# Kernel tuning notes

Hardware: AMD Instinct MI355X
Metric: run time of the kernel (lower is better)

## Reference

```python
import jax, jax.numpy as jnp
import numpy as np

LAYERS = [3, 1024, 512, 256, 128, 1]
WIDTHS = [3, 1024, 1024, 1024, 1024, 1]  # width per BsPINN: 2^(i-1)*Layers[i]
N = 131072


def _mask(num_blocks, bs1, bs2):
    # block-diagonal mask of ones, built statically (constant under jit)
    return jnp.asarray(np.kron(np.eye(num_blocks, dtype=np.float32),
                               np.ones((bs1, bs2), dtype=np.float32)))


def _xavier(key, shape, fan_in, fan_out):
    lim = np.sqrt(6.0 / (fan_in + fan_out)).astype(np.float32)
    return jax.random.uniform(key, shape, jnp.float32, -lim, lim)


def setup_inputs() -> dict:
    key = jax.random.key(0)
    ks = jax.random.split(key, 6)
    inp = {
        "X": jax.random.uniform(ks[0], (N, 3), dtype=jnp.float32),
        "lb_X": jnp.zeros((3,), jnp.float32),
        "ub_X": jnp.ones((3,), jnp.float32),
    }
    for i in range(5):
        # xavier scale per sub-block Layers[i] x Layers[i+1], as in the torch init
        inp[f"W{i}"] = _xavier(ks[i + 1], (WIDTHS[i], WIDTHS[i + 1]),
                               LAYERS[i], LAYERS[i + 1])
        inp[f"b{i}"] = jnp.zeros((1, WIDTHS[i + 1]), jnp.float32)
    return inp


def reference(X, lb_X, ub_X, W0, b0, W1, b1, W2, b2, W3, b3, W4, b4):
    # masks for hidden layers l=2,3: 2 blocks of 512x512, 4 blocks of 256x256
    m2 = _mask(2, LAYERS[2], 2 * LAYERS[3])   # [1024,1024]
    m3 = _mask(4, LAYERS[3], 2 * LAYERS[4])   # [1024,1024]
    h = 2.0 * (X - lb_X) / (ub_X - lb_X) - 1.0  # [N,3]
    h = jnp.sin(h @ W0 + b0)            # [N,1024] dense
    h = jnp.sin(h @ W1 + b1)            # [N,1024] dense
    h = jnp.sin(h @ (W2 * m2) + b2)     # [N,1024] block-diag (2 blocks)
    h = jnp.sin(h @ (W3 * m3) + b3)     # [N,1024] block-diag (4 blocks)
    return h @ W4 + b4                  # [N,1]
```

## Files before the change

kernel.cpp:

```cpp
#include <hip/hip_runtime.h>

typedef _Float16 f16x8 __attribute__((ext_vector_type(8)));
typedef _Float16 f16x4 __attribute__((ext_vector_type(4)));
typedef __fp16  fp16x2 __attribute__((ext_vector_type(2)));
typedef float f32x4 __attribute__((ext_vector_type(4)));
typedef unsigned int u32;

#define ROWS 64
#define THREADS 1024

__global__ __launch_bounds__(512) void pack_weights(
    const float* __restrict__ W1, const float* __restrict__ W2,
    const float* __restrict__ W3, _Float16* __restrict__ WF1,
    _Float16* __restrict__ WF2, _Float16* __restrict__ WF3) {
  int t = blockIdx.x * 512 + threadIdx.x;
  const float* src; _Float16* dst; int idx, ct, kt, lane, kbase;
  if (t < 131072) {
    idx = t; src = W1; dst = WF1;
    ct = idx >> 11; kt = (idx >> 6) & 31; lane = idx & 63; kbase = 0;
  } else if (t < 196608) {
    idx = t - 131072; src = W2; dst = WF2;
    ct = idx >> 10; kt = (idx >> 6) & 15; lane = idx & 63;
    kbase = (ct >= 32) ? 512 : 0;
  } else {
    idx = t - 196608; src = W3; dst = WF3;
    ct = idx >> 9; kt = (idx >> 6) & 7; lane = idx & 63;
    kbase = (ct >> 4) << 8;
  }
  int c  = ct * 16 + (lane & 15);
  int k0 = kbase + kt * 32 + ((lane >> 4) << 3);
  f16x8 v;
#pragma unroll
  for (int j = 0; j < 8; ++j) v[j] = (_Float16)src[(size_t)(k0 + j) * 1024 + c];
  *reinterpret_cast<f16x8*>(dst + (size_t)idx * 8) = v;
}

template <int KT>
__device__ __forceinline__ void layer_mfma(char* hb, const _Float16* __restrict__ WF,
                                           const float* __restrict__ bias,
                                           int wid, int lane, int kbase) {
  f32x4 acc[4][4];
#pragma unroll
  for (int cf = 0; cf < 4; ++cf)
#pragma unroll
    for (int rf = 0; rf < 4; ++rf) acc[cf][rf] = f32x4{0.f, 0.f, 0.f, 0.f};

  const f16x8* wf = reinterpret_cast<const f16x8*>(WF) +
                    (u32)(wid * 4 * KT * 64 + lane);
  const int arow = lane & 15;
  const int koff = (lane >> 4) << 3;
  const u32 abase = (u32)(arow * 2048);
  const u32 axor  = (u32)((arow & 7) << 4);

#pragma unroll 1
  for (int kt = 0; kt < KT; ++kt) {
    f16x8 w[4];
#pragma unroll
    for (int cf = 0; cf < 4; ++cf)
      w[cf] = wf[(u32)(cf * KT) * 64u + (u32)kt * 64u];
    u32 kb = (u32)((kbase + kt * 32 + koff) * 2);
    f16x8 h[4];
#pragma unroll
    for (int rf = 0; rf < 4; ++rf) {
      u32 addr = ((u32)(rf * 32768) + abase + kb) ^ axor;
      h[rf] = *reinterpret_cast<const f16x8*>(hb + addr);
    }
    __builtin_amdgcn_s_setprio(1);
#pragma unroll
    for (int cf = 0; cf < 4; ++cf)
#pragma unroll
      for (int rf = 0; rf < 4; ++rf)
        acc[cf][rf] = __builtin_amdgcn_mfma_f32_16x16x32_f16(w[cf], h[rf],
                                                             acc[cf][rf], 0, 0, 0);
    __builtin_amdgcn_s_setprio(0);
  }

  __syncthreads();
  const int csub = (lane >> 4) << 2;
  const int rr   = lane & 15;
#pragma unroll
  for (int cf = 0; cf < 4; ++cf) {
    int c0 = wid * 64 + cf * 16 + csub;
    f32x4 bb = *reinterpret_cast<const f32x4*>(bias + c0);
#pragma unroll
    for (int rf = 0; rf < 4; ++rf) {
      int r = rf * 16 + rr;
      float s0 = __sinf(acc[cf][rf][0] + bb[0]);
      float s1 = __sinf(acc[cf][rf][1] + bb[1]);
      float s2 = __sinf(acc[cf][rf][2] + bb[2]);
      float s3 = __sinf(acc[cf][rf][3] + bb[3]);
      union { fp16x2 h2[2]; f16x4 v; } pk;
      pk.h2[0] = __builtin_amdgcn_cvt_pkrtz(s0, s1);
      pk.h2[1] = __builtin_amdgcn_cvt_pkrtz(s2, s3);
      u32 addr = ((u32)(r * 2048 + c0 * 2)) ^ ((u32)((r & 7) << 4));
      *reinterpret_cast<f16x4*>(hb + addr) = pk.v;
    }
  }
  __syncthreads();
}

__global__
__attribute__((amdgpu_flat_work_group_size(1024, 1024), amdgpu_waves_per_eu(4, 4)))
void bspinn_fused(
    const float* __restrict__ X, const float* __restrict__ lb,
    const float* __restrict__ ub,
    const float* __restrict__ W0, const float* __restrict__ b0,
    const _Float16* __restrict__ WF1, const float* __restrict__ b1,
    const _Float16* __restrict__ WF2, const float* __restrict__ b2,
    const _Float16* __restrict__ WF3, const float* __restrict__ b3,
    const float* __restrict__ W4, const float* __restrict__ b4,
    float* __restrict__ out) {
  __shared__ alignas(16) char hb[ROWS * 2048];
  __shared__ float xs[ROWS * 4];
  __shared__ float partials[16 * ROWS];

  const int tid  = threadIdx.x;
  const int lane = tid & 63;
  const int wid  = tid >> 6;
  const int r0   = blockIdx.x * ROWS;

  if (tid < ROWS * 3) {
    int r = tid / 3, j = tid - r * 3;
    float x = X[(size_t)r0 * 3 + tid];
    xs[r * 4 + j] = 2.0f * (x - lb[j]) / (ub[j] - lb[j]) - 1.0f;
  }
  __syncthreads();

  {
    int c0 = tid;
    float wa0 = W0[c0];
    float wa1 = W0[1024 + c0];
    float wa2 = W0[2048 + c0];
    float ba = b0[c0];
#pragma unroll 4
    for (int r = 0; r < ROWS; ++r) {
      float x0 = xs[r * 4], x1 = xs[r * 4 + 1], x2 = xs[r * 4 + 2];
      float va = __sinf(fmaf(x2, wa2, fmaf(x1, wa1, fmaf(x0, wa0, ba))));
      u32 addr = ((u32)(r * 2048 + c0 * 2)) ^ ((u32)((r & 7) << 4));
      *reinterpret_cast<_Float16*>(hb + addr) = (_Float16)va;
    }
  }
  __syncthreads();

  layer_mfma<32>(hb, WF1, b1, wid, lane, 0);
  layer_mfma<16>(hb, WF2, b2, wid, lane, (wid >> 3) * 512);
  layer_mfma<8 >(hb, WF3, b3, wid, lane, (wid >> 2) * 256);

  {
    int r = lane, seg = wid;
    u32 rb = (u32)(r * 2048);
    u32 xr = (u32)((r & 7) << 4);
    float s = 0.f;
#pragma unroll
    for (int kk = 0; kk < 64; kk += 8) {
      int k = seg * 64 + kk;
      f16x8 v = *reinterpret_cast<const f16x8*>(hb + ((rb + (u32)(k * 2)) ^ xr));
#pragma unroll
      for (int j = 0; j < 8; ++j) s = fmaf((float)v[j], W4[k + j], s);
    }
    partials[seg * 64 + r] = s;
  }
  __syncthreads();
  if (tid < ROWS) {
    float s = b4[0];
#pragma unroll
    for (int g = 0; g < 16; ++g) s += partials[g * 64 + tid];
    out[r0 + tid] = s;
  }
}

extern "C" void kernel_launch(void* const* d_in, const int* in_sizes, int n_in,
                              void* d_out, int out_size, void* d_ws, size_t ws_size,
                              hipStream_t stream) {
  const float* X  = (const float*)d_in[0];
  const float* lb = (const float*)d_in[1];
  const float* ub = (const float*)d_in[2];
  const float* W0 = (const float*)d_in[3];
  const float* b0 = (const float*)d_in[4];
  const float* W1 = (const float*)d_in[5];
  const float* b1 = (const float*)d_in[6];
  const float* W2 = (const float*)d_in[7];
  const float* b2 = (const float*)d_in[8];
  const float* W3 = (const float*)d_in[9];
  const float* b3 = (const float*)d_in[10];
  const float* W4 = (const float*)d_in[11];
  const float* b4 = (const float*)d_in[12];
  float* out = (float*)d_out;

  _Float16* WF1 = (_Float16*)d_ws;
  _Float16* WF2 = (_Float16*)((char*)d_ws + 2097152);
  _Float16* WF3 = (_Float16*)((char*)d_ws + 2097152 + 1048576);

  hipLaunchKernelGGL(pack_weights, dim3(448), dim3(512), 0, stream,
                     W1, W2, W3, WF1, WF2, WF3);
  hipLaunchKernelGGL(bspinn_fused, dim3(131072 / ROWS), dim3(THREADS), 0, stream,
                     X, lb, ub, W0, b0, WF1, b1, WF2, b2, WF3, b3, W4, b4, out);
}
```

Measured before the change: 497.7 us.

## Split output columns across block pairs with 128-row tiles and native revolution sin

Each 128-row tile is now handled by two workgroups, each computing half of the 1024 hidden columns. The block-diagonal structure of layers 3 and 4 means each half only needs its own inputs, so the LDS activation buffer is 512 columns by 128 rows. The dense layer 2 is computed over two K halves, recomputing the cheap 3-input first layer for each half. This doubles the rows that reuse each weight fragment, cutting weight traffic per row. Sin now uses the hardware revolution-based sin with fract range reduction and 1/(2π) prescaling. In exchange there is redundant first-layer work, more barriers, a partial-sum buffer in workspace, and an extra reduce kernel launch.

```diff
diff --git a/kernel.cpp b/kernel.cpp
--- a/kernel.cpp
+++ b/kernel.cpp
@@ -6,8 +6,12 @@
 typedef float f32x4 __attribute__((ext_vector_type(4)));
 typedef unsigned int u32;
 
-#define ROWS 64
-#define THREADS 1024
+#define N_TOTAL 131072
+#define INV2PI 0.15915494309189535f
+
+__device__ __forceinline__ float fast_sin_revs(float t) {
+  return __builtin_amdgcn_sinf(__builtin_amdgcn_fractf(t));
+}
 
 __global__ __launch_bounds__(512) void pack_weights(
     const float* __restrict__ W1, const float* __restrict__ W2,
@@ -35,35 +39,28 @@
   *reinterpret_cast<f16x8*>(dst + (size_t)idx * 8) = v;
 }
 
-template <int KT>
-__device__ __forceinline__ void layer_mfma(char* hb, const _Float16* __restrict__ WF,
-                                           const float* __restrict__ bias,
-                                           int wid, int lane, int kbase) {
-  f32x4 acc[4][4];
-#pragma unroll
-  for (int cf = 0; cf < 4; ++cf)
-#pragma unroll
-    for (int rf = 0; rf < 4; ++rf) acc[cf][rf] = f32x4{0.f, 0.f, 0.f, 0.f};
-
-  const f16x8* wf = reinterpret_cast<const f16x8*>(WF) +
-                    (u32)(wid * 4 * KT * 64 + lane);
+template <int KTFULL>
+__device__ __forceinline__ void kloop(const _Float16* __restrict__ WF, char* hbr,
+                                      f32x4 (&acc)[4][4], int ct0, int lane,
+                                      int nkt, int ktW0, u32 ldsk0) {
+  const f16x8* wf = reinterpret_cast<const f16x8*>(WF);
   const int arow = lane & 15;
   const int koff = (lane >> 4) << 3;
-  const u32 abase = (u32)(arow * 2048);
+  const u32 abase = (u32)(arow * 1024);
   const u32 axor  = (u32)((arow & 7) << 4);
-
+  const u32 wbase = (u32)((ct0 * KTFULL + ktW0) * 64 + lane);
 #pragma unroll 1
-  for (int kt = 0; kt < KT; ++kt) {
+  for (int kt = 0; kt < nkt; ++kt) {
     f16x8 w[4];
 #pragma unroll
     for (int cf = 0; cf < 4; ++cf)
-      w[cf] = wf[(u32)(cf * KT) * 64u + (u32)kt * 64u];
-    u32 kb = (u32)((kbase + kt * 32 + koff) * 2);
+      w[cf] = wf[wbase + (u32)(cf * KTFULL) * 64u + (u32)kt * 64u];
+    u32 kb = ldsk0 + (u32)(kt * 64) + (u32)(koff * 2);
     f16x8 h[4];
 #pragma unroll
     for (int rf = 0; rf < 4; ++rf) {
-      u32 addr = ((u32)(rf * 32768) + abase + kb) ^ axor;
-      h[rf] = *reinterpret_cast<const f16x8*>(hb + addr);
+      u32 addr = ((u32)(rf * 16384) + abase + kb) ^ axor;
+      h[rf] = *reinterpret_cast<const f16x8*>(hbr + addr);
     }
     __builtin_amdgcn_s_setprio(1);
 #pragma unroll
@@ -74,29 +71,6 @@
                                                              acc[cf][rf], 0, 0, 0);
     __builtin_amdgcn_s_setprio(0);
   }
-
-  __syncthreads();
-  const int csub = (lane >> 4) << 2;
-  const int rr   = lane & 15;
-#pragma unroll
-  for (int cf = 0; cf < 4; ++cf) {
-    int c0 = wid * 64 + cf * 16 + csub;
-    f32x4 bb = *reinterpret_cast<const f32x4*>(bias + c0);
-#pragma unroll
-    for (int rf = 0; rf < 4; ++rf) {
-      int r = rf * 16 + rr;
-      float s0 = __sinf(acc[cf][rf][0] + bb[0]);
-      float s1 = __sinf(acc[cf][rf][1] + bb[1]);
-      float s2 = __sinf(acc[cf][rf][2] + bb[2]);
-      float s3 = __sinf(acc[cf][rf][3] + bb[3]);
-      union { fp16x2 h2[2]; f16x4 v; } pk;
-      pk.h2[0] = __builtin_amdgcn_cvt_pkrtz(s0, s1);
-      pk.h2[1] = __builtin_amdgcn_cvt_pkrtz(s2, s3);
-      u32 addr = ((u32)(r * 2048 + c0 * 2)) ^ ((u32)((r & 7) << 4));
-      *reinterpret_cast<f16x4*>(hb + addr) = pk.v;
-    }
-  }
-  __syncthreads();
 }
 
 __global__
@@ -108,65 +82,140 @@
     const _Float16* __restrict__ WF1, const float* __restrict__ b1,
     const _Float16* __restrict__ WF2, const float* __restrict__ b2,
     const _Float16* __restrict__ WF3, const float* __restrict__ b3,
-    const float* __restrict__ W4, const float* __restrict__ b4,
-    float* __restrict__ out) {
-  __shared__ alignas(16) char hb[ROWS * 2048];
-  __shared__ float xs[ROWS * 4];
-  __shared__ float partials[16 * ROWS];
+    const float* __restrict__ W4, float* __restrict__ P) {
+  __shared__ alignas(16) char hb[128 * 1024];
+  __shared__ float xs[128 * 4];
+  __shared__ float partials[16 * 128];
 
   const int tid  = threadIdx.x;
   const int lane = tid & 63;
   const int wid  = tid >> 6;
-  const int r0   = blockIdx.x * ROWS;
-
-  if (tid < ROWS * 3) {
+  const int tile = blockIdx.x >> 1;
+  const int half = blockIdx.x & 1;
+  const int r0   = tile * 128;
+
+  if (tid < 384) {
     int r = tid / 3, j = tid - r * 3;
     float x = X[(size_t)r0 * 3 + tid];
     xs[r * 4 + j] = 2.0f * (x - lb[j]) / (ub[j] - lb[j]) - 1.0f;
   }
+
+  const int cwave = wid & 7;
+  const int rgrp  = wid >> 3;
+  char* hbr = hb + rgrp * (64 * 1024);
+  const int ct0 = half * 32 + cwave * 4;
+
+  auto layer1 = [&](int cbase) {
+    int c1 = tid & 511;
+    int rb = (tid >> 9) * 64;
+    int cg = cbase + c1;
+    float w0v = W0[cg] * INV2PI, w1v = W0[1024 + cg] * INV2PI;
+    float w2v = W0[2048 + cg] * INV2PI, bv = b0[cg] * INV2PI;
+#pragma unroll 4
+    for (int rr = 0; rr < 64; ++rr) {
+      int r = rb + rr;
+      float x0 = xs[r * 4], x1 = xs[r * 4 + 1], x2 = xs[r * 4 + 2];
+      float v = fast_sin_revs(fmaf(x2, w2v, fmaf(x1, w1v, fmaf(x0, w0v, bv))));
+      u32 addr = ((u32)(r * 1024 + c1 * 2)) ^ ((u32)((r & 7) << 4));
+      *reinterpret_cast<_Float16*>(hb + addr) = (_Float16)v;
+    }
+  };
+
+  f32x4 acc[4][4];
+  auto zacc = [&]() {
+#pragma unroll
+    for (int cf = 0; cf < 4; ++cf)
+#pragma unroll
+      for (int rf = 0; rf < 4; ++rf) acc[cf][rf] = f32x4{0.f, 0.f, 0.f, 0.f};
+  };
+
+  auto epi = [&](const float* bias) {
+    const int csub = (lane >> 4) << 2;
+    const int rr = lane & 15;
+#pragma unroll
+    for (int cf = 0; cf < 4; ++cf) {
+      int cg = half * 512 + cwave * 64 + cf * 16 + csub;
+      int cl = cwave * 64 + cf * 16 + csub;
+      f32x4 bb = *reinterpret_cast<const f32x4*>(bias + cg);
+      f32x4 bc;
+#pragma unroll
+      for (int i = 0; i < 4; ++i) bc[i] = bb[i] * INV2PI;
+#pragma unroll
+      for (int rf = 0; rf < 4; ++rf) {
+        int r = rf * 16 + rr;
+        float s0 = fast_sin_revs(fmaf(acc[cf][rf][0], INV2PI, bc[0]));
+        float s1 = fast_sin_revs(fmaf(acc[cf][rf][1], INV2PI, bc[1]));
+        float s2 = fast_sin_revs(fmaf(acc[cf][rf][2], INV2PI, bc[2]));
+        float s3 = fast_sin_revs(fmaf(acc[cf][rf][3], INV2PI, bc[3]));
+        union { fp16x2 h2[2]; f16x4 v; } pk;
+        pk.h2[0] = __builtin_amdgcn_cvt_pkrtz(s0, s1);
+        pk.h2[1] = __builtin_amdgcn_cvt_pkrtz(s2, s3);
+        u32 addr = ((u32)(r * 1024 + cl * 2)) ^ ((u32)((r & 7) << 4));
+        *reinterpret_cast<f16x4*>(hbr + addr) = pk.v;
+      }
+    }
+  };
+
+  __syncthreads();
+  layer1(0);
+  __syncthreads();
+
+  zacc();
+  kloop<32>(WF1, hbr, acc, ct0, lane, 16, 0, 0);
+  __syncthreads();
+  layer1(512);
+  __syncthreads();
+  kloop<32>(WF1, hbr, acc, ct0, lane, 16, 16, 0);
+  __syncthreads();
+  epi(b1);
+  __syncthreads();
+
+  zacc();
+  kloop<16>(WF2, hbr, acc, ct0, lane, 16, 0, 0);
+  __syncthreads();
+  epi(b2);
+  __syncthreads();
+
+  zacc();
+  kloop<8>(WF3, hbr, acc, ct0, lane, 8, 0, (u32)((cwave >> 2) * 512));
+  __syncthreads();
+  epi(b3);
   __syncthreads();
 
   {
-    int c0 = tid;
-    float wa0 = W0[c0];
-    float wa1 = W0[1024 + c0];
-    float wa2 = W0[2048 + c0];
-    float ba = b0[c0];
-#pragma unroll 4
-    for (int r = 0; r < ROWS; ++r) {
-      float x0 = xs[r * 4], x1 = xs[r * 4 + 1], x2 = xs[r * 4 + 2];
-      float va = __sinf(fmaf(x2, wa2, fmaf(x1, wa1, fmaf(x0, wa0, ba))));
-      u32 addr = ((u32)(r * 2048 + c0 * 2)) ^ ((u32)((r & 7) << 4));
-      *reinterpret_cast<_Float16*>(hb + addr) = (_Float16)va;
-    }
-  }
-  __syncthreads();
-
-  layer_mfma<32>(hb, WF1, b1, wid, lane, 0);
-  layer_mfma<16>(hb, WF2, b2, wid, lane, (wid >> 3) * 512);
-  layer_mfma<8 >(hb, WF3, b3, wid, lane, (wid >> 2) * 256);
-
-  {
-    int r = lane, seg = wid;
-    u32 rb = (u32)(r * 2048);
-    u32 xr = (u32)((r & 7) << 4);
+    int seg = wid;
+    u32 xr = (u32)((lane & 7) << 4);
+    float s0 = 0.f, s1 = 0.f;
+#pragma unroll
+    for (int kk = 0; kk < 32; kk += 8) {
+      int kl = seg * 32 + kk;
+      const float* w4p = W4 + half * 512 + kl;
+      f16x8 v0 = *reinterpret_cast<const f16x8*>(hb + (((u32)(lane * 1024 + kl * 2)) ^ xr));
+      f16x8 v1 = *reinterpret_cast<const f16x8*>(hb + (((u32)((lane + 64) * 1024 + kl * 2)) ^ xr));
+#pragma unroll
+      for (int j = 0; j < 8; ++j) {
+        float wv = w4p[j];
+        s0 = fmaf((float)v0[j], wv, s0);
+        s1 = fmaf((float)v1[j], wv, s1);
+      }
+    }
+    partials[seg * 128 + lane]      = s0;
+    partials[seg * 128 + lane + 64] = s1;
+  }
+  __syncthreads();
+  if (tid < 128) {
     float s = 0.f;
 #pragma unroll
-    for (int kk = 0; kk < 64; kk += 8) {
-      int k = seg * 64 + kk;
-      f16x8 v = *reinterpret_cast<const f16x8*>(hb + ((rb + (u32)(k * 2)) ^ xr));
-#pragma unroll
-      for (int j = 0; j < 8; ++j) s = fmaf((float)v[j], W4[k + j], s);
-    }
-    partials[seg * 64 + r] = s;
-  }
-  __syncthreads();
-  if (tid < ROWS) {
-    float s = b4[0];
-#pragma unroll
-    for (int g = 0; g < 16; ++g) s += partials[g * 64 + tid];
-    out[r0 + tid] = s;
-  }
+    for (int g = 0; g < 16; ++g) s += partials[g * 128 + tid];
+    P[(size_t)half * N_TOTAL + r0 + tid] = s;
+  }
+}
+
+__global__ __launch_bounds__(256) void reduce_out(
+    const float* __restrict__ P, const float* __restrict__ b4,
+    float* __restrict__ out) {
+  int i = blockIdx.x * 256 + threadIdx.x;
+  out[i] = P[i] + P[N_TOTAL + i] + b4[0];
 }
 
 extern "C" void kernel_launch(void* const* d_in, const int* in_sizes, int n_in,
@@ -189,10 +238,13 @@
 
   _Float16* WF1 = (_Float16*)d_ws;
   _Float16* WF2 = (_Float16*)((char*)d_ws + 2097152);
-  _Float16* WF3 = (_Float16*)((char*)d_ws + 2097152 + 1048576);
+  _Float16* WF3 = (_Float16*)((char*)d_ws + 3145728);
+  float*    P   = (float*)((char*)d_ws + 3670016);
 
   hipLaunchKernelGGL(pack_weights, dim3(448), dim3(512), 0, stream,
                      W1, W2, W3, WF1, WF2, WF3);
-  hipLaunchKernelGGL(bspinn_fused, dim3(131072 / ROWS), dim3(THREADS), 0, stream,
-                     X, lb, ub, W0, b0, WF1, b1, WF2, b2, WF3, b3, W4, b4, out);
-}
+  hipLaunchKernelGGL(bspinn_fused, dim3((N_TOTAL / 128) * 2), dim3(1024), 0, stream,
+                     X, lb, ub, W0, b0, WF1, b1, WF2, b2, WF3, b3, W4, P);
+  hipLaunchKernelGGL(reduce_out, dim3(N_TOTAL / 256), dim3(256), 0, stream,
+                     P, b4, out);
+}
```

Measured after the change: 528.7 us. +6.2%, slower.
